# Optimization experiments

Hardware: AMD Instinct MI355X
Metric: run time of the kernel (lower is better)

## Reference

```python
import jax, jax.numpy as jnp
import numpy as np
import math

IN_DIM = 256
DQK = IN_DIM // 8


def setup_inputs() -> dict:
    key = jax.random.key(0)
    k = jax.random.split(key, 7)
    B, C, W = 4, IN_DIM, 4096
    x_0 = jax.random.normal(k[0], (B, C, W), dtype=jnp.float32)
    x_1 = jax.random.normal(k[1], (B, C, W), dtype=jnp.float32)
    s = 1.0 / math.sqrt(C)
    # 1x1 Conv1d == dense projection over channel dim: weight [out, in], bias [out]
    wq = jax.random.normal(k[2], (DQK, C), dtype=jnp.float32) * s
    bq = jax.random.normal(k[3], (DQK,), dtype=jnp.float32) * s
    wk = jax.random.normal(k[4], (DQK, C), dtype=jnp.float32) * s
    bk = jax.random.normal(k[5], (DQK,), dtype=jnp.float32) * s
    # torch init is zeros; use small random so the attention path contributes
    gamma = jax.random.normal(k[6], (1,), dtype=jnp.float32) * 0.1
    return {"x_0": x_0, "x_1": x_1, "wq": wq, "bq": bq, "wk": wk, "bk": bk, "gamma": gamma}


def reference(x_0, x_1, wq, bq, wk, bk, gamma):
    B, C, W0 = x_0.shape
    scale = 1.0 / math.sqrt(C)
    # 1x1 conv projections: [B, dqk, W]
    q = jnp.einsum('dc,bcw->bdw', wq, x_0) + bq[None, :, None]   # [B, dqk, W0]
    k = jnp.einsum('dc,bcw->bdw', wk, x_1) + bk[None, :, None]   # [B, dqk, W1]
    # energy = key^T @ query, scaled: [B, W1, W0]
    energy = jnp.einsum('bdm,bdn->bmn', k, q) * scale
    attention = jax.nn.softmax(energy, axis=-1)                  # softmax over W0
    # out = attention @ x_0^T -> [B, W1, C] -> permute to [B, C, W1]
    out = jnp.einsum('bmn,bcn->bcm', attention, x_0)
    out = gamma[0] * out + x_1
    return out, attention
```

## Files before the change

kernel.cpp:

```cpp
#include <hip/hip_runtime.h>
#include <stdint.h>

#define B_    4
#define C_    256
#define W_    4096
#define DQK_  32
#define NT64_ 64
#define TSZ_  16384

typedef short bf16x8 __attribute__((ext_vector_type(8)));
typedef float f32x4  __attribute__((ext_vector_type(4)));

__device__ __forceinline__ float fexp2f(float x){
#if __has_builtin(__builtin_amdgcn_exp2f)
  return __builtin_amdgcn_exp2f(x);
#else
  return exp2f(x);
#endif
}
__device__ __forceinline__ float frcpf(float x){
#if __has_builtin(__builtin_amdgcn_rcpf)
  return __builtin_amdgcn_rcpf(x);
#else
  return 1.0f / x;
#endif
}
__device__ __forceinline__ uint32_t cvtpk(float a, float b){
  uint32_t r;
  asm("v_cvt_pk_bf16_f32 %0, %1, %2" : "=v"(r) : "v"(a), "v"(b));
  return r;
}
__device__ __forceinline__ unsigned short bf16c(float f){
  return (unsigned short)cvtpk(f, f);
}

__global__ __launch_bounds__(512) void sa_prep(
    const float* __restrict__ x0, const float* __restrict__ x1,
    const float* __restrict__ wq, const float* __restrict__ bq,
    const float* __restrict__ wk, const float* __restrict__ bk,
    unsigned short* __restrict__ qf, unsigned short* __restrict__ kT,
    unsigned short* __restrict__ x0f)
{
  const int b     = blockIdx.y;
  const int tid   = threadIdx.x;
  const int lane  = tid & 63;
  const int cq    = tid >> 6;
  const int wloc  = lane & 31;
  const int chalf = lane >> 5;
  const int n0    = blockIdx.x * 32;
  const int n     = n0 + wloc;
  const int c0    = cq * 32 + chalf * 16;
  const size_t bw = (size_t)b * ((size_t)C_ * W_) + n;

  __shared__ union {
    unsigned short xs[256 * 32];
    float red[8][32][36];
  } sm;

  float accq[DQK_], acck[DQK_];
  #pragma unroll
  for (int d = 0; d < DQK_; ++d){ accq[d] = 0.f; acck[d] = 0.f; }

  for (int i = 0; i < 16; ++i){
    const int c = c0 + i;
    const size_t off = bw + (size_t)c * W_;
    const float v0 = x0[off];
    const float v1 = x1[off];
    sm.xs[c * 32 + wloc] = bf16c(v0);
    #pragma unroll
    for (int d = 0; d < DQK_; ++d){
      accq[d] = fmaf(wq[d * C_ + c], v0, accq[d]);
      acck[d] = fmaf(wk[d * C_ + c], v1, acck[d]);
    }
  }
  #pragma unroll
  for (int d = 0; d < DQK_; ++d){
    accq[d] += __shfl_xor(accq[d], 32);
    acck[d] += __shfl_xor(acck[d], 32);
  }
  __syncthreads();

  {
    unsigned short* xt = x0f + (size_t)(b * NT64_ + (n0 >> 6)) * TSZ_;
    const int ks = (n0 >> 5) & 1;
    const int wb = tid >> 6;
    const int lr2 = lane & 15, lg2 = lane >> 4;
    #pragma unroll
    for (int ct = 0; ct < 2; ++ct){
      uint4 v = *(const uint4*)&sm.xs[(wb * 32 + ct * 16 + lr2) * 32 + lg2 * 8];
      *(uint4*)(xt + ((size_t)(wb * 4 + ct * 2 + ks) * 64 + lane) * 8) = v;
    }
  }
  __syncthreads();

  if (chalf == 0){
    #pragma unroll
    for (int d4 = 0; d4 < 8; ++d4){
      f32x4 t = { accq[d4*4], accq[d4*4+1], accq[d4*4+2], accq[d4*4+3] };
      *(f32x4*)&sm.red[cq][wloc][d4 * 4] = t;
    }
  }
  __syncthreads();
  if (tid < 256){
    const int nl = tid & 31, dg = tid >> 5;
    const int d0 = dg * 4;
    float s[4];
    #pragma unroll
    for (int j = 0; j < 4; ++j){
      float t = bq[d0 + j];
      #pragma unroll
      for (int g = 0; g < 8; ++g) t += sm.red[g][nl][d0 + j];
      s[j] = t;
    }
    uint2 pk; pk.x = cvtpk(s[0], s[1]); pk.y = cvtpk(s[2], s[3]);
    const int ng = n0 + nl;
    const size_t addr = (((size_t)b * 256 + (ng >> 4)) * 64
                         + (ng & 15) + ((dg >> 1) << 4)) * 8 + (dg & 1) * 4;
    *(uint2*)(qf + addr) = pk;
  }
  __syncthreads();

  if (chalf == 0){
    #pragma unroll
    for (int d4 = 0; d4 < 8; ++d4){
      f32x4 t = { acck[d4*4], acck[d4*4+1], acck[d4*4+2], acck[d4*4+3] };
      *(f32x4*)&sm.red[cq][wloc][d4 * 4] = t;
    }
  }
  __syncthreads();
  if (tid < 256){
    const float SCL = 0.0625f * 1.44269504088896340736f;
    const int nl = tid & 31, dg = tid >> 5;
    const int d0 = dg * 4;
    float s[4];
    #pragma unroll
    for (int j = 0; j < 4; ++j){
      float t = bk[d0 + j];
      #pragma unroll
      for (int g = 0; g < 8; ++g) t += sm.red[g][nl][d0 + j];
      s[j] = t * SCL;
    }
    uint2 pk; pk.x = cvtpk(s[0], s[1]); pk.y = cvtpk(s[2], s[3]);
    *(uint2*)(kT + ((size_t)b * W_ + n0 + nl) * DQK_ + d0) = pk;
  }
}

__global__ __launch_bounds__(512, 4) void sa_fused(
    const unsigned short* __restrict__ qf, const unsigned short* __restrict__ kT,
    const unsigned short* __restrict__ x0f, const float* __restrict__ x1,
    const float* __restrict__ gamma,
    float* __restrict__ out, float* __restrict__ att)
{
  const int lb = blockIdx.x;
  const int b    = (lb & 7) >> 1;
  const int mblk = ((lb >> 3) << 1) | (lb & 1);
  const int m0 = mblk * 32;
  const int tid = threadIdx.x;
  const int lane = tid & 63;
  const int wid = tid >> 6;
  const int lr = lane & 15, lg = lane >> 4;
  const int mt = wid & 1, nq = wid >> 1;

  __shared__ __align__(16) unsigned short Plds[2][32 * 64];
  __shared__ float ssum[8][16];

  const bf16x8 kf = *(const bf16x8*)(kT + ((size_t)b * W_ + m0 + mt * 16 + lr) * DQK_ + lg * 8);
  const unsigned short* qfw = qf + ((size_t)b * 256 * 64 + (size_t)nq * 64 + lane) * 8;
  const unsigned short* afw = x0f + (size_t)b * NT64_ * TSZ_ + wid * 2048 + lane * 8;

  float ps = 0.f;
  {
    const unsigned short* qp = qfw + 2048;
    bf16x8 qv = *(const bf16x8*)qfw;
    for (int s = 0; s < NT64_; ++s){
      bf16x8 qn = *(const bf16x8*)qp;
      qp = (s == NT64_ - 2) ? qfw : (qp + 2048);
      f32x4 e = __builtin_amdgcn_mfma_f32_16x16x32_bf16(qv, kf, (f32x4){0.f,0.f,0.f,0.f}, 0, 0, 0);
      ps += fexp2f(e[0]) + fexp2f(e[1]) + fexp2f(e[2]) + fexp2f(e[3]);
      qv = qn;
    }
  }
  ps += __shfl_xor(ps, 16);
  ps += __shfl_xor(ps, 32);
  if (lane < 16) ssum[wid][lane] = ps;
  __syncthreads();
  const float is = frcpf(ssum[mt][lr] + ssum[mt + 2][lr] + ssum[mt + 4][lr] + ssum[mt + 6][lr]);

  f32x4 acc[2][2];
  #pragma unroll
  for (int ct = 0; ct < 2; ++ct)
    #pragma unroll
    for (int m2 = 0; m2 < 2; ++m2) acc[ct][m2] = (f32x4){0.f,0.f,0.f,0.f};

  const int mlocP = mt * 16 + lr;
  const int pw_off = mlocP * 64
      + (((nq * 2 + (lg >> 1)) ^ (mlocP & 7)) << 3) + (lg & 1) * 4;
  int pfo[2][2];
  #pragma unroll
  for (int m2 = 0; m2 < 2; ++m2){
    const int prow = m2 * 16 + lr;
    #pragma unroll
    for (int ks = 0; ks < 2; ++ks)
      pfo[m2][ks] = prow * 64 + (((ks * 4 + lg) ^ (prow & 7)) << 3);
  }

  const unsigned short* qp = qfw + 2048;
  const unsigned short* afp = afw + TSZ_;
  float* attw = att + ((size_t)b * W_ + m0 + mt * 16 + lr) * W_ + nq * 16 + lg * 4;

  bf16x8 qv = *(const bf16x8*)qfw;
  bf16x8 af0 = *(const bf16x8*)(afw);
  bf16x8 af1 = *(const bf16x8*)(afw + 512);
  bf16x8 af2 = *(const bf16x8*)(afw + 1024);
  bf16x8 af3 = *(const bf16x8*)(afw + 1536);

  for (int s = 0; s < NT64_; ++s){
    const int cur = s & 1;

    f32x4 e = __builtin_amdgcn_mfma_f32_16x16x32_bf16(qv, kf, (f32x4){0.f,0.f,0.f,0.f}, 0, 0, 0);
    f32x4 p;
    #pragma unroll
    for (int r = 0; r < 4; ++r) p[r] = fexp2f(e[r]) * is;
    uint2 pv; pv.x = cvtpk(p[0], p[1]); pv.y = cvtpk(p[2], p[3]);
    *(uint2*)(&Plds[cur][0] + pw_off) = pv;

    asm volatile("s_waitcnt lgkmcnt(0)" ::: "memory");
    __builtin_amdgcn_sched_barrier(0);
    __builtin_amdgcn_s_barrier();

    qv = *(const bf16x8*)qp;
    qp = (s == NT64_ - 2) ? qfw : (qp + 2048);
    bf16x8 an0 = *(const bf16x8*)(afp);
    bf16x8 an1 = *(const bf16x8*)(afp + 512);
    bf16x8 an2 = *(const bf16x8*)(afp + 1024);
    bf16x8 an3 = *(const bf16x8*)(afp + 1536);
    afp = (s == NT64_ - 2) ? afw : (afp + TSZ_);
    __builtin_nontemporal_store(p, (f32x4*)attw);
    attw += 64;

    const unsigned short* Pb = &Plds[cur][0];
    bf16x8 pf[2][2];
    __builtin_amdgcn_s_setprio(1);
    #pragma unroll
    for (int m2 = 0; m2 < 2; ++m2)
      #pragma unroll
      for (int ks = 0; ks < 2; ++ks)
        pf[m2][ks] = *(const bf16x8*)(Pb + pfo[m2][ks]);
    acc[0][0] = __builtin_amdgcn_mfma_f32_16x16x32_bf16(af0, pf[0][0], acc[0][0], 0, 0, 0);
    acc[0][1] = __builtin_amdgcn_mfma_f32_16x16x32_bf16(af0, pf[1][0], acc[0][1], 0, 0, 0);
    acc[0][0] = __builtin_amdgcn_mfma_f32_16x16x32_bf16(af1, pf[0][1], acc[0][0], 0, 0, 0);
    acc[0][1] = __builtin_amdgcn_mfma_f32_16x16x32_bf16(af1, pf[1][1], acc[0][1], 0, 0, 0);
    acc[1][0] = __builtin_amdgcn_mfma_f32_16x16x32_bf16(af2, pf[0][0], acc[1][0], 0, 0, 0);
    acc[1][1] = __builtin_amdgcn_mfma_f32_16x16x32_bf16(af2, pf[1][0], acc[1][1], 0, 0, 0);
    acc[1][0] = __builtin_amdgcn_mfma_f32_16x16x32_bf16(af3, pf[0][1], acc[1][0], 0, 0, 0);
    acc[1][1] = __builtin_amdgcn_mfma_f32_16x16x32_bf16(af3, pf[1][1], acc[1][1], 0, 0, 0);
    __builtin_amdgcn_s_setprio(0);

    af0 = an0; af1 = an1; af2 = an2; af3 = an3;
  }

  const float g = gamma[0];
  const float* x1b = x1 + (size_t)b * C_ * W_;
  float* outb = out + (size_t)b * C_ * W_;
  #pragma unroll
  for (int ct = 0; ct < 2; ++ct)
    #pragma unroll
    for (int m2 = 0; m2 < 2; ++m2)
      #pragma unroll
      for (int r = 0; r < 4; ++r){
        const int c = wid * 32 + ct * 16 + lg * 4 + r;
        const size_t idx = (size_t)c * W_ + m0 + m2 * 16 + lr;
        const float xv = __builtin_nontemporal_load(&x1b[idx]);
        __builtin_nontemporal_store(fmaf(g, acc[ct][m2][r], xv), &outb[idx]);
      }
}

extern "C" void kernel_launch(void* const* d_in, const int* in_sizes, int n_in,
                              void* d_out, int out_size, void* d_ws, size_t ws_size,
                              hipStream_t stream)
{
  (void)in_sizes; (void)n_in; (void)out_size; (void)ws_size;
  const float* x0    = (const float*)d_in[0];
  const float* x1    = (const float*)d_in[1];
  const float* wq    = (const float*)d_in[2];
  const float* bq    = (const float*)d_in[3];
  const float* wk    = (const float*)d_in[4];
  const float* bk    = (const float*)d_in[5];
  const float* gamma = (const float*)d_in[6];

  unsigned short* qf  = (unsigned short*)d_ws;
  unsigned short* kT  = qf + (size_t)B_ * W_ * DQK_;
  unsigned short* x0f = kT + (size_t)B_ * W_ * DQK_;

  float* out = (float*)d_out;
  float* att = out + (size_t)B_ * C_ * W_;

  sa_prep <<<dim3(128, 4), 512, 0, stream>>>(x0, x1, wq, bq, wk, bk, qf, kT, x0f);
  sa_fused<<<512, 512, 0, stream>>>(qf, kT, x0f, x1, gamma, out, att);
}
```

Measured before the change: 155.3 us.

## Widen prep kernel tile to 64 columns per block, drop cross-half shuffle reduction

The projection prep kernel now handles 64 width positions per block, with each wave covering 32 channels for all 64 lanes. This removes the xor-shuffle reduction across lane halves and lets each block write a full 64-wide x0 bf16 tile. The shared-memory layouts are padded to 68 and 33 to avoid bank conflicts. The grid halves to 256 blocks, which lowers parallelism for the prep stage while each thread runs twice as many channel iterations.

```diff
diff --git a/kernel.cpp b/kernel.cpp
--- a/kernel.cpp
+++ b/kernel.cpp
@@ -41,68 +41,55 @@
     unsigned short* __restrict__ qf, unsigned short* __restrict__ kT,
     unsigned short* __restrict__ x0f)
 {
-  const int b     = blockIdx.y;
-  const int tid   = threadIdx.x;
-  const int lane  = tid & 63;
-  const int cq    = tid >> 6;
-  const int wloc  = lane & 31;
-  const int chalf = lane >> 5;
-  const int n0    = blockIdx.x * 32;
-  const int n     = n0 + wloc;
-  const int c0    = cq * 32 + chalf * 16;
+  const int b    = blockIdx.y;
+  const int nt   = blockIdx.x;
+  const int tid  = threadIdx.x;
+  const int lane = tid & 63;
+  const int cq   = __builtin_amdgcn_readfirstlane(tid >> 6);
+  const int n    = nt * 64 + lane;
+  const int lr   = lane & 15, lg = lane >> 4;
   const size_t bw = (size_t)b * ((size_t)C_ * W_) + n;
 
   __shared__ union {
-    unsigned short xs[256 * 32];
-    float red[8][32][36];
+    unsigned short xs[256 * 68];
+    float red[8][64][33];
   } sm;
 
   float accq[DQK_], acck[DQK_];
   #pragma unroll
   for (int d = 0; d < DQK_; ++d){ accq[d] = 0.f; acck[d] = 0.f; }
 
-  for (int i = 0; i < 16; ++i){
+  const int c0 = cq * 32;
+  for (int i = 0; i < 32; ++i){
     const int c = c0 + i;
     const size_t off = bw + (size_t)c * W_;
     const float v0 = x0[off];
     const float v1 = x1[off];
-    sm.xs[c * 32 + wloc] = bf16c(v0);
+    sm.xs[c * 68 + lane] = bf16c(v0);
     #pragma unroll
     for (int d = 0; d < DQK_; ++d){
       accq[d] = fmaf(wq[d * C_ + c], v0, accq[d]);
       acck[d] = fmaf(wk[d * C_ + c], v1, acck[d]);
     }
   }
-  #pragma unroll
-  for (int d = 0; d < DQK_; ++d){
-    accq[d] += __shfl_xor(accq[d], 32);
-    acck[d] += __shfl_xor(acck[d], 32);
-  }
-  __syncthreads();
-
-  {
-    unsigned short* xt = x0f + (size_t)(b * NT64_ + (n0 >> 6)) * TSZ_;
-    const int ks = (n0 >> 5) & 1;
-    const int wb = tid >> 6;
-    const int lr2 = lane & 15, lg2 = lane >> 4;
-    #pragma unroll
-    for (int ct = 0; ct < 2; ++ct){
-      uint4 v = *(const uint4*)&sm.xs[(wb * 32 + ct * 16 + lr2) * 32 + lg2 * 8];
-      *(uint4*)(xt + ((size_t)(wb * 4 + ct * 2 + ks) * 64 + lane) * 8) = v;
-    }
-  }
-  __syncthreads();
-
-  if (chalf == 0){
-    #pragma unroll
-    for (int d4 = 0; d4 < 8; ++d4){
-      f32x4 t = { accq[d4*4], accq[d4*4+1], accq[d4*4+2], accq[d4*4+3] };
-      *(f32x4*)&sm.red[cq][wloc][d4 * 4] = t;
-    }
-  }
-  __syncthreads();
-  if (tid < 256){
-    const int nl = tid & 31, dg = tid >> 5;
+
+  {
+    unsigned short* xt = x0f + (size_t)(b * NT64_ + nt) * TSZ_;
+    #pragma unroll
+    for (int ct = 0; ct < 2; ++ct)
+      #pragma unroll
+      for (int ks = 0; ks < 2; ++ks){
+        uint4 v = *(const uint4*)&sm.xs[(c0 + ct * 16 + lr) * 68 + ks * 32 + lg * 8];
+        *(uint4*)(xt + ((size_t)((cq * 2 + ct) * 2 + ks) * 64 + lane) * 8) = v;
+      }
+  }
+  __syncthreads();
+
+  #pragma unroll
+  for (int d = 0; d < DQK_; ++d) sm.red[cq][lane][d] = accq[d];
+  __syncthreads();
+  {
+    const int nl = tid & 63, dg = tid >> 6;
     const int d0 = dg * 4;
     float s[4];
     #pragma unroll
@@ -113,24 +100,19 @@
       s[j] = t;
     }
     uint2 pk; pk.x = cvtpk(s[0], s[1]); pk.y = cvtpk(s[2], s[3]);
-    const int ng = n0 + nl;
+    const int ng = nt * 64 + nl;
     const size_t addr = (((size_t)b * 256 + (ng >> 4)) * 64
                          + (ng & 15) + ((dg >> 1) << 4)) * 8 + (dg & 1) * 4;
     *(uint2*)(qf + addr) = pk;
   }
   __syncthreads();
 
-  if (chalf == 0){
-    #pragma unroll
-    for (int d4 = 0; d4 < 8; ++d4){
-      f32x4 t = { acck[d4*4], acck[d4*4+1], acck[d4*4+2], acck[d4*4+3] };
-      *(f32x4*)&sm.red[cq][wloc][d4 * 4] = t;
-    }
-  }
-  __syncthreads();
-  if (tid < 256){
+  #pragma unroll
+  for (int d = 0; d < DQK_; ++d) sm.red[cq][lane][d] = acck[d];
+  __syncthreads();
+  {
     const float SCL = 0.0625f * 1.44269504088896340736f;
-    const int nl = tid & 31, dg = tid >> 5;
+    const int nl = tid & 63, dg = tid >> 6;
     const int d0 = dg * 4;
     float s[4];
     #pragma unroll
@@ -141,7 +123,7 @@
       s[j] = t * SCL;
     }
     uint2 pk; pk.x = cvtpk(s[0], s[1]); pk.y = cvtpk(s[2], s[3]);
-    *(uint2*)(kT + ((size_t)b * W_ + n0 + nl) * DQK_ + d0) = pk;
+    *(uint2*)(kT + ((size_t)b * W_ + nt * 64 + nl) * DQK_ + d0) = pk;
   }
 }
 
@@ -295,6 +277,6 @@
   float* out = (float*)d_out;
   float* att = out + (size_t)B_ * C_ * W_;
 
-  sa_prep <<<dim3(128, 4), 512, 0, stream>>>(x0, x1, wq, bq, wk, bk, qf, kT, x0f);
+  sa_prep <<<dim3(64, 4), 512, 0, stream>>>(x0, x1, wq, bq, wk, bk, qf, kT, x0f);
   sa_fused<<<512, 512, 0, stream>>>(qf, kT, x0f, x1, gamma, out, att);
 }
```

After: 128.4 us. -17.3%, faster.
